# Kernel tuning notes

Hardware: AMD Instinct MI355X
Metric: run time of the kernel (lower is better)

The kernel has to match this reference:

```python
import jax, jax.numpy as jnp
import numpy as np
from jax import lax


def setup_inputs() -> dict:
    key = jax.random.key(0)
    k1, k2 = jax.random.split(key)
    B, N, C, H, W = 4, 32, 32, 64, 64
    x = jax.random.normal(k1, (B, N, C, H, W), dtype=jnp.float32)
    # grouped conv weight: groups = N*C, 1 input channel per group, 3 outputs per group
    w = jax.random.normal(k2, (3 * N * C, 1, 1, 1), dtype=jnp.float32) * 0.1
    return {"x": x, "w": w}


def reference(x, w):
    B, N, C, H, W = x.shape
    xc = x.reshape(B, N * C, H, W)
    # grouped 1x1 conv (groups = N*C), matches nn.Conv2d(inC*N, 3*qkvC*N, 1, groups=qkvC*N, bias=False)
    qkv = lax.conv_general_dilated(
        xc, w,
        window_strides=(1, 1), padding=[(0, 0), (0, 0)],
        feature_group_count=N * C,
        dimension_numbers=("NCHW", "OIHW", "NCHW"),
    )
    qkv = qkv.reshape(B, N, C, 3, H, W)
    scale = (H * W) ** (-0.5)
    q = scale * qkv[:, :, :, 0]           # (B,N,C,H,W)
    k = qkv[:, :, :, 1]
    v = qkv[:, :, :, 2]
    # original: 6D einsum (a,b,c,d,e,f) then sum over d,e == contraction over H,W
    S = jnp.einsum("bachw,bfchw->bcaf", q, k)   # (B,C,N,N)
    A = jax.nn.softmax(S, axis=-1)
    # original: broadcast-multiply with v and sum over f
    out = jnp.einsum("bcaf,bfchw->abchw", A, v)  # (N,B,C,H,W)
    return out
```

## Files before the change

### kernel.cpp

```cpp
#include <hip/hip_runtime.h>

#define BB 4
#define NN 32
#define CC 32
#define HWD 4096
#define SPLIT 4
#define CHUNK 1024
#define SUB 128

__device__ __forceinline__ void gld_lds16(float* lds, const float* g) {
    __builtin_amdgcn_global_load_lds(
        (const __attribute__((address_space(1))) void*)g,
        (__attribute__((address_space(3))) void*)lds,
        16, 0, 0);
}

__global__ __launch_bounds__(256) void k_gram(const float* __restrict__ x,
                                              float* __restrict__ Gp) {
    const int bid = blockIdx.x;
    const int s   = bid & (SPLIT - 1);
    const int bc  = bid >> 2;
    const int b   = bc >> 5, c = bc & 31;
    const int tid = threadIdx.x;
    const int wv  = tid >> 6;
    const int pos = tid & 63;
    const int pa  = pos >> 3;
    const int pf  = pos & 7;

    __shared__ __align__(16) float tile[SUB][36];
    __shared__ __align__(16) float red[4 * 64 * 16];

    const float* xb = x + ((size_t)(b * NN) * CC + c) * HWD + s * CHUNK;
    const size_t arow = (size_t)CC * HWD;

    float acc[4][4];
#pragma unroll
    for (int i = 0; i < 4; ++i)
#pragma unroll
        for (int j = 0; j < 4; ++j) acc[i][j] = 0.f;

    const int la = tid >> 3;
    const int t7 = tid & 7;

    for (int ch = 0; ch < CHUNK / SUB; ++ch) {
        __syncthreads();
#pragma unroll
        for (int k = 0; k < 4; ++k) {
            const int q = t7 + 8 * k;
            const float4 v = *(const float4*)(xb + (size_t)la * arow + ch * SUB + 4 * q);
            tile[4 * q + 0][la] = v.x;
            tile[4 * q + 1][la] = v.y;
            tile[4 * q + 2][la] = v.z;
            tile[4 * q + 3][la] = v.w;
        }
        __syncthreads();
#pragma unroll 8
        for (int h = 0; h < 32; ++h) {
            const int hw = wv * 32 + h;
            const float4 va = *(const float4*)&tile[hw][4 * pa];
            const float4 vf = *(const float4*)&tile[hw][4 * pf];
            float xa[4] = {va.x, va.y, va.z, va.w};
            float xf[4] = {vf.x, vf.y, vf.z, vf.w};
#pragma unroll
            for (int i = 0; i < 4; ++i)
#pragma unroll
                for (int j = 0; j < 4; ++j)
                    acc[i][j] = fmaf(xa[i], xf[j], acc[i][j]);
        }
    }

#pragma unroll
    for (int i = 0; i < 4; ++i)
#pragma unroll
        for (int j = 0; j < 4; ++j)
            red[wv * 1024 + pos * 16 + i * 4 + j] = acc[i][j];
    __syncthreads();

    const int t   = tid;
    const int pa2 = t >> 5;
    const int i2  = (t >> 3) & 3;
    const int pf2 = t & 7;
    const int P   = (pa2 * 8 + pf2) * 16 + i2 * 4;
    float4 sum = make_float4(0.f, 0.f, 0.f, 0.f);
#pragma unroll
    for (int w2 = 0; w2 < 4; ++w2) {
        const float4 v = *(const float4*)&red[w2 * 1024 + P];
        sum.x += v.x; sum.y += v.y; sum.z += v.z; sum.w += v.w;
    }
    *(float4*)&Gp[(size_t)bid * 1024 + 4 * t] = sum;
}

__global__ __launch_bounds__(64) void k_softmax(const float* __restrict__ Gp,
                                                const float* __restrict__ w,
                                                float* __restrict__ Ahat) {
    const int bc = blockIdx.x;
    const int c  = bc & 31;
    const int a  = threadIdx.x;
    if (a >= 32) return;

    const float wq = w[(a * CC + c) * 3 + 0] * 0.015625f;
    float S[32];
#pragma unroll
    for (int f = 0; f < 32; ++f) {
        float g = 0.f;
#pragma unroll
        for (int s = 0; s < SPLIT; ++s)
            g += Gp[(size_t)(bc * SPLIT + s) * 1024 + a * 32 + f];
        const float wk = w[(f * CC + c) * 3 + 1];
        S[f] = wq * wk * g;
    }
    float m = S[0];
#pragma unroll
    for (int f = 1; f < 32; ++f) m = fmaxf(m, S[f]);
    float sum = 0.f;
#pragma unroll
    for (int f = 0; f < 32; ++f) { S[f] = __expf(S[f] - m); sum += S[f]; }
    const float inv = 1.f / sum;
#pragma unroll
    for (int f = 0; f < 32; ++f) {
        const float wvv = w[(f * CC + c) * 3 + 2];
        Ahat[(size_t)bc * 1024 + a * 32 + f] = S[f] * inv * wvv;
    }
}

__global__ __launch_bounds__(256) void k_pv(const float* __restrict__ x,
                                            const float* __restrict__ Ahat,
                                            float* __restrict__ out) {
    const int bid = blockIdx.x;
    const int ch  = bid & 15;
    const int bc  = bid >> 4;
    const int b   = bc >> 5, c = bc & 31;
    const int tid = threadIdx.x;
    const int wv  = tid >> 6;
    const int ln  = tid & 63;
    const int q   = ln;

    __shared__ __align__(16) float XL[32][256];
    __shared__ __align__(16) float AL[1024];

    const float* xbase = x + ((size_t)(b * NN) * CC + c) * HWD + ch * 256;
    const size_t frow = (size_t)CC * HWD;
#pragma unroll
    for (int k = 0; k < 8; ++k) {
        const int f = k * 4 + wv;
        gld_lds16(&XL[f][0], xbase + (size_t)f * frow + ln * 4);
    }
    gld_lds16(&AL[wv * 256], Ahat + (size_t)bc * 1024 + wv * 256 + ln * 4);
    __syncthreads();

    float acc[8][4];
#pragma unroll
    for (int i = 0; i < 8; ++i)
#pragma unroll
        for (int j = 0; j < 4; ++j) acc[i][j] = 0.f;

#pragma unroll
    for (int f = 0; f < 32; ++f) {
        const float4 xv = *(const float4*)&XL[f][4 * q];
#pragma unroll
        for (int i = 0; i < 8; ++i) {
            const float av = AL[(8 * wv + i) * 32 + f];
            acc[i][0] = fmaf(av, xv.x, acc[i][0]);
            acc[i][1] = fmaf(av, xv.y, acc[i][1]);
            acc[i][2] = fmaf(av, xv.z, acc[i][2]);
            acc[i][3] = fmaf(av, xv.w, acc[i][3]);
        }
    }

#pragma unroll
    for (int i = 0; i < 8; ++i) {
        const int a = 8 * wv + i;
        const float4 v = make_float4(acc[i][0], acc[i][1], acc[i][2], acc[i][3]);
        *(float4*)(out + (((size_t)a * BB + b) * CC + c) * HWD + ch * 256 + 4 * q) = v;
    }
}

extern "C" void kernel_launch(void* const* d_in, const int* in_sizes, int n_in,
                              void* d_out, int out_size, void* d_ws, size_t ws_size,
                              hipStream_t stream) {
    const float* x = (const float*)d_in[0];
    const float* w = (const float*)d_in[1];
    float* outp = (float*)d_out;
    float* Gp   = (float*)d_ws;
    float* Ahat = Gp + (size_t)512 * 1024;

    hipLaunchKernelGGL(k_gram,    dim3(512),  dim3(256), 0, stream, x, Gp);
    hipLaunchKernelGGL(k_softmax, dim3(128),  dim3(64),  0, stream, Gp, w, Ahat);
    hipLaunchKernelGGL(k_pv,      dim3(2048), dim3(256), 0, stream, x, Ahat, outp);
}
```

Measured before the change: 53.08 us.

## Use bf16 MFMA for Gram and PV matmuls, parallelize softmax across lanes

```diff
diff --git a/kernel.cpp b/kernel.cpp
--- a/kernel.cpp
+++ b/kernel.cpp
@@ -1,177 +1,166 @@
 #include <hip/hip_runtime.h>
+
+typedef __attribute__((ext_vector_type(8))) short bf16x8;
+typedef __attribute__((ext_vector_type(4))) float f32x4;
 
 #define BB 4
 #define NN 32
 #define CC 32
 #define HWD 4096
-#define SPLIT 4
-#define CHUNK 1024
-#define SUB 128
+#define AROW ((size_t)CC * HWD)
 
-__device__ __forceinline__ void gld_lds16(float* lds, const float* g) {
-    __builtin_amdgcn_global_load_lds(
-        (const __attribute__((address_space(1))) void*)g,
-        (__attribute__((address_space(3))) void*)lds,
-        16, 0, 0);
+__device__ __forceinline__ unsigned cvt_pk_bf16(float lo, float hi) {
+    unsigned r;
+    asm("v_cvt_pk_bf16_f32 %0, %1, %2" : "=v"(r) : "v"(lo), "v"(hi));
+    return r;
+}
+
+__device__ __forceinline__ bf16x8 pack8(float4 a, float4 b) {
+    union { unsigned u[4]; bf16x8 v; } u;
+    u.u[0] = cvt_pk_bf16(a.x, a.y);
+    u.u[1] = cvt_pk_bf16(a.z, a.w);
+    u.u[2] = cvt_pk_bf16(b.x, b.y);
+    u.u[3] = cvt_pk_bf16(b.z, b.w);
+    return u.v;
 }
 
 __global__ __launch_bounds__(256) void k_gram(const float* __restrict__ x,
                                               float* __restrict__ Gp) {
     const int bid = blockIdx.x;
-    const int s   = bid & (SPLIT - 1);
-    const int bc  = bid >> 2;
+    const int s   = bid & 7;
+    const int bc  = bid >> 3;
     const int b   = bc >> 5, c = bc & 31;
     const int tid = threadIdx.x;
-    const int wv  = tid >> 6;
-    const int pos = tid & 63;
-    const int pa  = pos >> 3;
-    const int pf  = pos & 7;
+    const int w   = tid >> 6, l = tid & 63;
+    const int r   = l & 15, g = l >> 4;
 
-    __shared__ __align__(16) float tile[SUB][36];
-    __shared__ __align__(16) float red[4 * 64 * 16];
+    const float* xb = x + ((size_t)b * NN * CC + c) * HWD;
+    const int hwbase = s * 512 + w * 128;
+    const float* p0 = xb + (size_t)r        * AROW + hwbase + 8 * g;
+    const float* p1 = xb + (size_t)(r + 16) * AROW + hwbase + 8 * g;
 
-    const float* xb = x + ((size_t)(b * NN) * CC + c) * HWD + s * CHUNK;
-    const size_t arow = (size_t)CC * HWD;
+    f32x4 acc[2][2];
+#pragma unroll
+    for (int i = 0; i < 2; ++i)
+#pragma unroll
+        for (int j = 0; j < 2; ++j)
+#pragma unroll
+            for (int q = 0; q < 4; ++q) acc[i][j][q] = 0.f;
 
-    float acc[4][4];
 #pragma unroll
-    for (int i = 0; i < 4; ++i)
-#pragma unroll
-        for (int j = 0; j < 4; ++j) acc[i][j] = 0.f;
-
-    const int la = tid >> 3;
-    const int t7 = tid & 7;
-
-    for (int ch = 0; ch < CHUNK / SUB; ++ch) {
-        __syncthreads();
-#pragma unroll
-        for (int k = 0; k < 4; ++k) {
-            const int q = t7 + 8 * k;
-            const float4 v = *(const float4*)(xb + (size_t)la * arow + ch * SUB + 4 * q);
-            tile[4 * q + 0][la] = v.x;
-            tile[4 * q + 1][la] = v.y;
-            tile[4 * q + 2][la] = v.z;
-            tile[4 * q + 3][la] = v.w;
-        }
-        __syncthreads();
-#pragma unroll 8
-        for (int h = 0; h < 32; ++h) {
-            const int hw = wv * 32 + h;
-            const float4 va = *(const float4*)&tile[hw][4 * pa];
-            const float4 vf = *(const float4*)&tile[hw][4 * pf];
-            float xa[4] = {va.x, va.y, va.z, va.w};
-            float xf[4] = {vf.x, vf.y, vf.z, vf.w};
-#pragma unroll
-            for (int i = 0; i < 4; ++i)
-#pragma unroll
-                for (int j = 0; j < 4; ++j)
-                    acc[i][j] = fmaf(xa[i], xf[j], acc[i][j]);
-        }
+    for (int ch = 0; ch < 4; ++ch) {
+        const float4 a0 = *(const float4*)(p0 + ch * 32);
+        const float4 a1 = *(const float4*)(p0 + ch * 32 + 4);
+        const float4 b0 = *(const float4*)(p1 + ch * 32);
+        const float4 b1 = *(const float4*)(p1 + ch * 32 + 4);
+        const bf16x8 F0 = pack8(a0, a1);
+        const bf16x8 F1 = pack8(b0, b1);
+        acc[0][0] = __builtin_amdgcn_mfma_f32_16x16x32_bf16(F0, F0, acc[0][0], 0, 0, 0);
+        acc[0][1] = __builtin_amdgcn_mfma_f32_16x16x32_bf16(F0, F1, acc[0][1], 0, 0, 0);
+        acc[1][0] = __builtin_amdgcn_mfma_f32_16x16x32_bf16(F1, F0, acc[1][0], 0, 0, 0);
+        acc[1][1] = __builtin_amdgcn_mfma_f32_16x16x32_bf16(F1, F1, acc[1][1], 0, 0, 0);
     }
 
+    __shared__ float red[4][64][16];
 #pragma unroll
-    for (int i = 0; i < 4; ++i)
+    for (int ta = 0; ta < 2; ++ta)
 #pragma unroll
-        for (int j = 0; j < 4; ++j)
-            red[wv * 1024 + pos * 16 + i * 4 + j] = acc[i][j];
+        for (int tf = 0; tf < 2; ++tf)
+#pragma unroll
+            for (int q = 0; q < 4; ++q)
+                red[w][l][(ta * 2 + tf) * 4 + q] = acc[ta][tf][q];
     __syncthreads();
 
-    const int t   = tid;
-    const int pa2 = t >> 5;
-    const int i2  = (t >> 3) & 3;
-    const int pf2 = t & 7;
-    const int P   = (pa2 * 8 + pf2) * 16 + i2 * 4;
-    float4 sum = make_float4(0.f, 0.f, 0.f, 0.f);
+    const int a   = tid >> 3;
+    const int f0  = 4 * (tid & 7);
+    const int lg  = ((a >> 2) & 3) * 16 + (f0 & 15);
+    const int reg = ((a >> 4) * 2 + (f0 >> 4)) * 4 + (a & 3);
+    float sv[4];
 #pragma unroll
-    for (int w2 = 0; w2 < 4; ++w2) {
-        const float4 v = *(const float4*)&red[w2 * 1024 + P];
-        sum.x += v.x; sum.y += v.y; sum.z += v.z; sum.w += v.w;
+    for (int j = 0; j < 4; ++j) {
+        float v = 0.f;
+#pragma unroll
+        for (int ww = 0; ww < 4; ++ww) v += red[ww][lg + j][reg];
+        sv[j] = v;
     }
-    *(float4*)&Gp[(size_t)bid * 1024 + 4 * t] = sum;
+    *(float4*)&Gp[(size_t)bid * 1024 + 4 * tid] = make_float4(sv[0], sv[1], sv[2], sv[3]);
 }
 
-__global__ __launch_bounds__(64) void k_softmax(const float* __restrict__ Gp,
-                                                const float* __restrict__ w,
-                                                float* __restrict__ Ahat) {
+__global__ __launch_bounds__(256) void k_softmax(const float* __restrict__ Gp,
+                                                 const float* __restrict__ w,
+                                                 unsigned short* __restrict__ Ahat) {
     const int bc = blockIdx.x;
     const int c  = bc & 31;
-    const int a  = threadIdx.x;
-    if (a >= 32) return;
+    const int t  = threadIdx.x;
+    const int a  = t >> 3, fo = 4 * (t & 7);
 
-    const float wq = w[(a * CC + c) * 3 + 0] * 0.015625f;
-    float S[32];
+    float gs[4] = {0.f, 0.f, 0.f, 0.f};
 #pragma unroll
-    for (int f = 0; f < 32; ++f) {
-        float g = 0.f;
+    for (int s = 0; s < 8; ++s) {
+        const float4 v = *(const float4*)&Gp[(size_t)(bc * 8 + s) * 1024 + a * 32 + fo];
+        gs[0] += v.x; gs[1] += v.y; gs[2] += v.z; gs[3] += v.w;
+    }
+    const float wq = w[(a * CC + c) * 3] * 0.015625f;
+    float S[4];
 #pragma unroll
-        for (int s = 0; s < SPLIT; ++s)
-            g += Gp[(size_t)(bc * SPLIT + s) * 1024 + a * 32 + f];
-        const float wk = w[(f * CC + c) * 3 + 1];
-        S[f] = wq * wk * g;
-    }
-    float m = S[0];
+    for (int j = 0; j < 4; ++j)
+        S[j] = wq * w[((fo + j) * CC + c) * 3 + 1] * gs[j];
+
+    float m = fmaxf(fmaxf(S[0], S[1]), fmaxf(S[2], S[3]));
 #pragma unroll
-    for (int f = 1; f < 32; ++f) m = fmaxf(m, S[f]);
-    float sum = 0.f;
+    for (int o = 1; o < 8; o <<= 1) m = fmaxf(m, __shfl_xor(m, o, 64));
+    float e[4], sum = 0.f;
 #pragma unroll
-    for (int f = 0; f < 32; ++f) { S[f] = __expf(S[f] - m); sum += S[f]; }
+    for (int j = 0; j < 4; ++j) { e[j] = __expf(S[j] - m); sum += e[j]; }
+#pragma unroll
+    for (int o = 1; o < 8; o <<= 1) sum += __shfl_xor(sum, o, 64);
     const float inv = 1.f / sum;
-#pragma unroll
-    for (int f = 0; f < 32; ++f) {
-        const float wvv = w[(f * CC + c) * 3 + 2];
-        Ahat[(size_t)bc * 1024 + a * 32 + f] = S[f] * inv * wvv;
-    }
+
+    float o0 = e[0] * inv * w[((fo + 0) * CC + c) * 3 + 2];
+    float o1 = e[1] * inv * w[((fo + 1) * CC + c) * 3 + 2];
+    float o2 = e[2] * inv * w[((fo + 2) * CC + c) * 3 + 2];
+    float o3 = e[3] * inv * w[((fo + 3) * CC + c) * 3 + 2];
+    uint2 pk = make_uint2(cvt_pk_bf16(o0, o1), cvt_pk_bf16(o2, o3));
+    *(uint2*)&Ahat[(size_t)bc * 1024 + a * 32 + fo] = pk;
 }
 
 __global__ __launch_bounds__(256) void k_pv(const float* __restrict__ x,
-                                            const float* __restrict__ Ahat,
+                                            const unsigned short* __restrict__ Ahat,
                                             float* __restrict__ out) {
-    const int bid = blockIdx.x;
-    const int ch  = bid & 15;
-    const int bc  = bid >> 4;
-    const int b   = bc >> 5, c = bc & 31;
-    const int tid = threadIdx.x;
-    const int wv  = tid >> 6;
-    const int ln  = tid & 63;
-    const int q   = ln;
+    const int bid   = blockIdx.x;
+    const int chunk = bid & 15;
+    const int bc    = bid >> 4;
+    const int b     = bc >> 5, c = bc & 31;
+    const int tid   = threadIdx.x;
+    const int w     = tid >> 6, l = tid & 63;
+    const int r     = l & 15, g = l >> 4;
 
-    __shared__ __align__(16) float XL[32][256];
-    __shared__ __align__(16) float AL[1024];
+    const unsigned short* ab = Ahat + (size_t)bc * 1024;
+    const bf16x8 A0 = *(const bf16x8*)(ab + r * 32 + 8 * g);
+    const bf16x8 A1 = *(const bf16x8*)(ab + (r + 16) * 32 + 8 * g);
 
-    const float* xbase = x + ((size_t)(b * NN) * CC + c) * HWD + ch * 256;
-    const size_t frow = (size_t)CC * HWD;
-#pragma unroll
-    for (int k = 0; k < 8; ++k) {
-        const int f = k * 4 + wv;
-        gld_lds16(&XL[f][0], xbase + (size_t)f * frow + ln * 4);
-    }
-    gld_lds16(&AL[wv * 256], Ahat + (size_t)bc * 1024 + wv * 256 + ln * 4);
-    __syncthreads();
-
-    float acc[8][4];
-#pragma unroll
-    for (int i = 0; i < 8; ++i)
-#pragma unroll
-        for (int j = 0; j < 4; ++j) acc[i][j] = 0.f;
+    const float* xb = x + ((size_t)b * NN * CC + c) * HWD + chunk * 256 + w * 64;
+    const f32x4 zero = {0.f, 0.f, 0.f, 0.f};
 
 #pragma unroll
-    for (int f = 0; f < 32; ++f) {
-        const float4 xv = *(const float4*)&XL[f][4 * q];
+    for (int ht = 0; ht < 4; ++ht) {
+        const int hw = ht * 16 + r;
+        const float* bp = xb + (size_t)(8 * g) * AROW + hw;
+        float bf[8];
 #pragma unroll
-        for (int i = 0; i < 8; ++i) {
-            const float av = AL[(8 * wv + i) * 32 + f];
-            acc[i][0] = fmaf(av, xv.x, acc[i][0]);
-            acc[i][1] = fmaf(av, xv.y, acc[i][1]);
-            acc[i][2] = fmaf(av, xv.z, acc[i][2]);
-            acc[i][3] = fmaf(av, xv.w, acc[i][3]);
+        for (int i = 0; i < 8; ++i) bf[i] = bp[(size_t)i * AROW];
+        const bf16x8 B = pack8(make_float4(bf[0], bf[1], bf[2], bf[3]),
+                               make_float4(bf[4], bf[5], bf[6], bf[7]));
+        f32x4 d0 = __builtin_amdgcn_mfma_f32_16x16x32_bf16(A0, B, zero, 0, 0, 0);
+        f32x4 d1 = __builtin_amdgcn_mfma_f32_16x16x32_bf16(A1, B, zero, 0, 0, 0);
+
+        const size_t hwg = (size_t)chunk * 256 + w * 64 + ht * 16 + r;
+#pragma unroll
+        for (int q = 0; q < 4; ++q) {
+            const int arow0 = g * 4 + q;
+            out[(((size_t)arow0 * BB + b) * CC + c) * HWD + hwg]        = d0[q];
+            out[(((size_t)(arow0 + 16) * BB + b) * CC + c) * HWD + hwg] = d1[q];
         }
-    }
-
-#pragma unroll
-    for (int i = 0; i < 8; ++i) {
-        const int a = 8 * wv + i;
-        const float4 v = make_float4(acc[i][0], acc[i][1], acc[i][2], acc[i][3]);
-        *(float4*)(out + (((size_t)a * BB + b) * CC + c) * HWD + ch * 256 + 4 * q) = v;
     }
 }
 
@@ -181,10 +170,10 @@
     const float* x = (const float*)d_in[0];
     const float* w = (const float*)d_in[1];
     float* outp = (float*)d_out;
-    float* Gp   = (float*)d_ws;
-    float* Ahat = Gp + (size_t)512 * 1024;
+    float* Gp = (float*)d_ws;
+    unsigned short* Ahat = (unsigned short*)((char*)d_ws + (size_t)4 * 1024 * 1024);
 
-    hipLaunchKernelGGL(k_gram,    dim3(512),  dim3(256), 0, stream, x, Gp);
-    hipLaunchKernelGGL(k_softmax, dim3(128),  dim3(64),  0, stream, Gp, w, Ahat);
+    hipLaunchKernelGGL(k_gram,    dim3(1024), dim3(256), 0, stream, x, Gp);
+    hipLaunchKernelGGL(k_softmax, dim3(128),  dim3(256), 0, stream, Gp, w, Ahat);
     hipLaunchKernelGGL(k_pv,      dim3(2048), dim3(256), 0, stream, x, Ahat, outp);
 }
```

New measurement: 44.18 us. -16.8%, faster.
